# Kernel optimization log

Measured on AMD Instinct MI355X. Metric: run time of the kernel, lower is better.

Reference implementation:

```python
import jax, jax.numpy as jnp
import numpy as np

EPSILON = 1e-8
MAX_WEIGHT = 0.15
N_ITER = 20
STEP_SIZE = 0.05
B, P = 32768, 45


def _simplex_projection(w):
    # clamp + renormalize, done twice (differentiable approximation)
    w = jnp.clip(w, 0.0, MAX_WEIGHT)
    w = w / (jnp.sum(w, axis=-1, keepdims=True) + EPSILON)
    w = jnp.clip(w, 0.0, MAX_WEIGHT)
    w = w / (jnp.sum(w, axis=-1, keepdims=True) + EPSILON)
    return w


def setup_inputs() -> dict:
    key = jax.random.key(0)
    k1, k2 = jax.random.split(key, 2)
    # SPD-ish covariance for a well-behaved iterative solve
    A = jax.random.normal(k1, (B, P, P), dtype=jnp.float32) * 0.1
    sigma = jnp.einsum('bij,bkj->bik', A, A) + 0.1 * jnp.eye(P, dtype=jnp.float32)
    beta = jax.nn.softmax(jax.random.normal(k2, (B, P), dtype=jnp.float32), axis=-1)
    w_prev = jnp.full((B, P), 1.0 / P, dtype=jnp.float32)
    return {
        'sigma': sigma,
        'beta': beta,
        'w_prev': w_prev,
        'log_lambda_sparse': jnp.asarray(-3.0, dtype=jnp.float32),
        'log_lambda_turnover': jnp.asarray(-2.0, dtype=jnp.float32),
    }


def reference(sigma, beta, w_prev, log_lambda_sparse, log_lambda_turnover):
    Bb, Pp = beta.shape
    lam_s = jnp.exp(log_lambda_sparse)
    lam_t = jnp.exp(log_lambda_turnover)
    w0 = jnp.full((Bb, Pp), 1.0 / Pp, dtype=sigma.dtype)

    def step(w, _):
        Sw = jnp.einsum('bij,bj->bi', sigma, w)  # [B,P]
        grad = 2.0 * Sw - beta + lam_s * jnp.sign(w) + 2.0 * lam_t * (w - w_prev)
        w = _simplex_projection(w - STEP_SIZE * grad)
        return w, None

    w, _ = jax.lax.scan(step, w0, None, length=N_ITER)
    return w
```

## Files before the change

kernel.cpp:

```cpp
#include <hip/hip_runtime.h>
#include <math.h>

#define P 45
#define N_ITER 20

template<int CTRL>
__device__ __forceinline__ float dpp_add(float x) {
    int xi = __builtin_bit_cast(int, x);
    int yi = __builtin_amdgcn_update_dpp(0, xi, CTRL, 0xF, 0xF, true);
    return x + __builtin_bit_cast(float, yi);
}

__device__ __forceinline__ float wave_sum_bcast(float x) {
    x = dpp_add<0x111>(x);
    x = dpp_add<0x112>(x);
    x = dpp_add<0x114>(x);
    x = dpp_add<0x118>(x);
    x = dpp_add<0x142>(x);
    x = dpp_add<0x143>(x);
    int si = __builtin_amdgcn_readlane(__builtin_bit_cast(int, x), 63);
    return __builtin_bit_cast(float, si);
}

__global__ __launch_bounds__(64, 4) void drb_kernel(
    const float* __restrict__ sigma,
    const float* __restrict__ beta,
    const float* __restrict__ w_prev,
    const float* __restrict__ lls,
    const float* __restrict__ llt,
    float* __restrict__ out)
{
    const int b    = blockIdx.x;
    const int lane = threadIdx.x;
    const bool active = lane < P;
    const int  c   = active ? lane : (P - 1);

    const float lam_s  = expf(lls[0]);
    const float lam_t2 = 2.0f * expf(llt[0]);

    const float* sp = sigma + (size_t)b * (P * P) + c;
    float row[P];
    #pragma unroll
    for (int j = 0; j < P; ++j) row[j] = sp[(size_t)j * P];
    #pragma unroll
    for (int j = 0; j < P; ++j) asm volatile("" : "+v"(row[j]));

    float bet = active ? beta[(size_t)b * P + lane]   : 0.0f;
    float wp  = active ? w_prev[(size_t)b * P + lane] : 0.0f;
    float wc  = active ? (float)(1.0 / 45.0)          : 0.0f;

    for (int it = 0; it < N_ITER; ++it) {
        const int wci = __builtin_bit_cast(int, wc);

        float ws[P];
        #pragma unroll
        for (int j = 0; j < P; ++j)
            ws[j] = __builtin_bit_cast(float, __builtin_amdgcn_readlane(wci, j));

        float acc0 = 0.0f, acc1 = 0.0f, acc2 = 0.0f;
        #pragma unroll
        for (int j = 0; j < P; j += 3) {
            acc0 = fmaf(row[j],     ws[j],     acc0);
            acc1 = fmaf(row[j + 1], ws[j + 1], acc1);
            acc2 = fmaf(row[j + 2], ws[j + 2], acc2);
        }
        const float acc = (acc0 + acc1) + acc2;

        float sgn = (wc > 0.0f) ? 1.0f : ((wc < 0.0f) ? -1.0f : 0.0f);
        float g   = 2.0f * acc - bet + lam_s * sgn + lam_t2 * (wc - wp);
        float wn  = wc - 0.05f * g;
        wn = active ? wn : 0.0f;

        wn = fminf(fmaxf(wn, 0.0f), 0.15f);
        float s = wave_sum_bcast(wn);
        wn *= __builtin_amdgcn_rcpf(s + 1e-8f);

        wn = fminf(fmaxf(wn, 0.0f), 0.15f);
        s = wave_sum_bcast(wn);
        wn *= __builtin_amdgcn_rcpf(s + 1e-8f);

        wc = wn;
    }

    if (active) out[(size_t)b * P + lane] = wc;
}

extern "C" void kernel_launch(void* const* d_in, const int* in_sizes, int n_in,
                              void* d_out, int out_size, void* d_ws, size_t ws_size,
                              hipStream_t stream) {
    const float* sigma  = (const float*)d_in[0];
    const float* beta   = (const float*)d_in[1];
    const float* w_prev = (const float*)d_in[2];
    const float* lls    = (const float*)d_in[3];
    const float* llt    = (const float*)d_in[4];
    float* out = (float*)d_out;

    const int B = in_sizes[1] / P;
    drb_kernel<<<B, 64, 0, stream>>>(sigma, beta, w_prev, lls, llt, out);
}
```

Before: 401.6 us.

## Defer final renormalization into next iteration, overlap its reduction with matvec

Keeps the weight unnormalized after the second clamp and carries it into the next iteration, where its sum is computed alongside the readlane broadcast and matrix-vector product. The normalization factor is folded algebraically into the gradient using linearity of the matvec. This moves one wave reduction off the serial critical path per iteration and uses fmed3 for the clamps. It also drops the min-waves launch bound hint and zeroes inactive rows. The reformulation changes rounding slightly and assumes weights stay nonnegative so that sign reduces to a positivity test.

```diff
diff --git a/kernel.cpp b/kernel.cpp
--- a/kernel.cpp
+++ b/kernel.cpp
@@ -22,7 +22,11 @@
     return __builtin_bit_cast(float, si);
 }
 
-__global__ __launch_bounds__(64, 4) void drb_kernel(
+__device__ __forceinline__ float clamp015(float x) {
+    return __builtin_amdgcn_fmed3f(x, 0.0f, 0.15f);
+}
+
+__global__ __launch_bounds__(64) void drb_kernel(
     const float* __restrict__ sigma,
     const float* __restrict__ beta,
     const float* __restrict__ w_prev,
@@ -33,56 +37,64 @@
     const int b    = blockIdx.x;
     const int lane = threadIdx.x;
     const bool active = lane < P;
-    const int  c   = active ? lane : (P - 1);
+    const int  cidx = active ? lane : (P - 1);
 
     const float lam_s  = expf(lls[0]);
     const float lam_t2 = 2.0f * expf(llt[0]);
 
-    const float* sp = sigma + (size_t)b * (P * P) + c;
+    float bet = active ? beta[(size_t)b * P + lane]   : 0.0f;
+    float wp  = active ? w_prev[(size_t)b * P + lane] : 0.0f;
+
+    const float* sp = sigma + (size_t)b * (P * P) + cidx;
     float row[P];
     #pragma unroll
-    for (int j = 0; j < P; ++j) row[j] = sp[(size_t)j * P];
+    for (int j = 0; j < P; ++j) {
+        float v = sp[(size_t)j * P];
+        row[j] = active ? v : 0.0f;
+    }
     #pragma unroll
     for (int j = 0; j < P; ++j) asm volatile("" : "+v"(row[j]));
 
-    float bet = active ? beta[(size_t)b * P + lane]   : 0.0f;
-    float wp  = active ? w_prev[(size_t)b * P + lane] : 0.0f;
-    float wc  = active ? (float)(1.0 / 45.0)          : 0.0f;
+    const float base = -bet - lam_t2 * wp;
+
+    float c = active ? (float)(1.0 / 45.0) : 0.0f;
 
     for (int it = 0; it < N_ITER; ++it) {
-        const int wci = __builtin_bit_cast(int, wc);
+        const int ci = __builtin_bit_cast(int, c);
 
-        float ws[P];
+        float cs[P];
         #pragma unroll
         for (int j = 0; j < P; ++j)
-            ws[j] = __builtin_bit_cast(float, __builtin_amdgcn_readlane(wci, j));
+            cs[j] = __builtin_bit_cast(float, __builtin_amdgcn_readlane(ci, j));
+
+        float s2 = wave_sum_bcast(c);
+        float r  = __builtin_amdgcn_rcpf(s2 + 1e-8f);
 
         float acc0 = 0.0f, acc1 = 0.0f, acc2 = 0.0f;
         #pragma unroll
         for (int j = 0; j < P; j += 3) {
-            acc0 = fmaf(row[j],     ws[j],     acc0);
-            acc1 = fmaf(row[j + 1], ws[j + 1], acc1);
-            acc2 = fmaf(row[j + 2], ws[j + 2], acc2);
+            acc0 = fmaf(row[j],     cs[j],     acc0);
+            acc1 = fmaf(row[j + 1], cs[j + 1], acc1);
+            acc2 = fmaf(row[j + 2], cs[j + 2], acc2);
         }
         const float acc = (acc0 + acc1) + acc2;
 
-        float sgn = (wc > 0.0f) ? 1.0f : ((wc < 0.0f) ? -1.0f : 0.0f);
-        float g   = 2.0f * acc - bet + lam_s * sgn + lam_t2 * (wc - wp);
-        float wn  = wc - 0.05f * g;
-        wn = active ? wn : 0.0f;
+        const float t  = c * r;
+        const float u  = r + r;
+        float g = fmaf(lam_t2, t, base);
+        g += (c > 0.0f) ? lam_s : 0.0f;
+        g  = fmaf(u, acc, g);
+        const float x = fmaf(-0.05f, g, t);
 
-        wn = fminf(fmaxf(wn, 0.0f), 0.15f);
-        float s = wave_sum_bcast(wn);
-        wn *= __builtin_amdgcn_rcpf(s + 1e-8f);
-
-        wn = fminf(fmaxf(wn, 0.0f), 0.15f);
-        s = wave_sum_bcast(wn);
-        wn *= __builtin_amdgcn_rcpf(s + 1e-8f);
-
-        wc = wn;
+        const float a  = clamp015(x);
+        const float s1 = wave_sum_bcast(a);
+        const float r1 = __builtin_amdgcn_rcpf(s1 + 1e-8f);
+        c = clamp015(a * r1);
     }
 
-    if (active) out[(size_t)b * P + lane] = wc;
+    const float sf = wave_sum_bcast(c);
+    const float rf = __builtin_amdgcn_rcpf(sf + 1e-8f);
+    if (active) out[(size_t)b * P + lane] = c * rf;
 }
 
 extern "C" void kernel_launch(void* const* d_in, const int* in_sizes, int n_in,
```

Measured after the change: 397.5 us. About the same (-1.0%).
